# Kernel tuning notes

Measured on AMD Instinct MI355X. Metric: run time of the kernel, lower is better.

Reference implementation:

```python
import jax, jax.numpy as jnp
import numpy as np
import math

B, H, L, D = 2, 16, 2048, 128

def setup_inputs() -> dict:
    key = jax.random.key(0)
    kq, kk, kv, km = jax.random.split(key, 4)
    q = jax.random.normal(kq, (B, H, L, D), dtype=jnp.float32)
    k = jax.random.normal(kk, (B, H, L, D), dtype=jnp.float32)
    v = jax.random.normal(kv, (B, H, L, D), dtype=jnp.float32)
    mask = jax.random.randint(km, (B, 1, L, L), 0, 2, dtype=jnp.int32)
    return {"q": q, "k": k, "v": v, "mask": mask}

def reference(q, k, v, mask):
    d_tensor = q.shape[-1]
    # ReLU applied to V before attention (the custom twist)
    v = jax.nn.relu(v)
    # score = q @ k^T / sqrt(d)  -> [B,H,L,L]
    score = jnp.einsum('bhqd,bhkd->bhqk', q, k) / math.sqrt(d_tensor)
    score = jnp.where(mask == 0, jnp.float32(-10000.0), score)
    attn = jax.nn.softmax(score, axis=-1)
    # result = attn @ relu(v) -> [B,H,L,D]
    return jnp.einsum('bhqk,bhkd->bhqd', attn, v)
```

## Files before the change

### kernel.cpp

```cpp
#include <hip/hip_runtime.h>
#include <hip/hip_bf16.h>
#include <math.h>

typedef __attribute__((ext_vector_type(8)))  short short8;
typedef __attribute__((ext_vector_type(16))) float f32x16;

#define Bc    2
#define Hc    16
#define Lc    2048
#define Dc    128
#define QBLK  128
#define KBLK  64
#define LOG2E 1.4426950408889634f
#define SCALE 0.08838834764831845f
#define SCL2  (SCALE * LOG2E)

#define KB_OFF   0u
#define KB_BYTES (32u * 2048u * 128u * 2u)
#define VT_OFF   (KB_OFF + KB_BYTES)
#define VT_BYTES (32u * 2048u * 128u * 2u)
#define MB_OFF   (VT_OFF + VT_BYTES)

__device__ __forceinline__ unsigned pk2(float a, float b) {
    unsigned short ua = __builtin_bit_cast(unsigned short, __float2bfloat16(a));
    unsigned short ub = __builtin_bit_cast(unsigned short, __float2bfloat16(b));
    return (unsigned)ua | ((unsigned)ub << 16);
}
__device__ __forceinline__ unsigned short bf16b(float a) {
    return __builtin_bit_cast(unsigned short, __float2bfloat16(a));
}
__device__ __forceinline__ void gload_lds16(const void* g, void* l) {
    __builtin_amdgcn_global_load_lds(
        (const __attribute__((address_space(1))) unsigned int*)g,
        (__attribute__((address_space(3))) unsigned int*)l, 16, 0, 0);
}
__device__ __forceinline__ unsigned cvtpk(float lo, float hi) {
    unsigned r;
    asm("v_cvt_pk_bf16_f32 %0, %1, %2" : "=v"(r) : "v"(lo), "v"(hi));
    return r;
}

__global__ void prepass_kernel(const float* __restrict__ k, const float* __restrict__ v,
                               const int* __restrict__ mask,
                               unsigned short* __restrict__ kb, unsigned short* __restrict__ vt,
                               unsigned long long* __restrict__ mb) {
    __shared__ float t[32][33];
    int bid = blockIdx.x;
    int tid = threadIdx.x;
    if (bid < 4096) {
        size_t base = ((size_t)bid * 256 + tid) * 8;
        float4 f0 = *(const float4*)(k + base);
        float4 f1 = *(const float4*)(k + base + 4);
        uint4 w;
        w.x = pk2(f0.x, f0.y); w.y = pk2(f0.z, f0.w);
        w.z = pk2(f1.x, f1.y); w.w = pk2(f1.z, f1.w);
        *(uint4*)(kb + base) = w;
    } else if (bid < 12288) {
        int b2 = bid - 4096;
        int bh = b2 >> 8, rem = b2 & 255;
        int l0 = (rem >> 2) * 32, d0 = (rem & 3) * 32;
        int tx = tid & 31, ty = tid >> 5;
        const float* src = v + (size_t)bh * Lc * Dc;
        unsigned short* dst = vt + (size_t)bh * Dc * Lc;
        #pragma unroll
        for (int i = 0; i < 4; ++i) {
            int row = ty * 4 + i;
            t[row][tx] = fmaxf(src[(size_t)(l0 + row) * Dc + d0 + tx], 0.f);
        }
        __syncthreads();
        #pragma unroll
        for (int i = 0; i < 4; ++i) {
            int drow = ty * 4 + i;
            dst[(size_t)(d0 + drow) * Lc + l0 + tx] = bf16b(t[tx][drow]);
        }
    } else {
        int m = bid - 12288;
        int wv = tid >> 6, lane = tid & 63;
        #pragma unroll
        for (int i = 0; i < 16; ++i) {
            int wid = m * 64 + wv * 16 + i;
            int b = wid >> 16, l = (wid >> 5) & 2047, ktw = wid & 31;
            int mm = mask[(((size_t)(b * 2048 + l)) << 11) + ktw * 64 + lane];
            unsigned long long bal = __ballot(mm != 0);
            if (lane == 0) mb[(((size_t)(b * 32 + ktw)) << 11) + l] = bal;
        }
    }
}

__global__ __launch_bounds__(256, 2) void rev_attn_kernel(
    const float* __restrict__ q,
    const unsigned short* __restrict__ kb,
    const unsigned short* __restrict__ vt,
    const unsigned long long* __restrict__ mb,
    float* __restrict__ out)
{
    __shared__ __align__(16) char smem[65536];

    const int tid  = threadIdx.x;
    const int w    = tid >> 6;
    const int lane = tid & 63;
    const int l31  = lane & 31;
    const int hi   = lane >> 5;
    const int bh   = blockIdx.y;
    const int b    = bh >> 4;
    const int qb   = blockIdx.x * QBLK + w * 32;
    const int qrow = qb + l31;

    const float*              qp = q  + (size_t)bh * Lc * Dc;
    const unsigned short*     kp = kb + (size_t)bh * Lc * Dc;
    const unsigned short*     vp = vt + (size_t)bh * Dc * Lc;
    const unsigned long long* mp = mb + ((size_t)b << 16);
    float*                    op = out + (size_t)bh * Lc * Dc;

    short8 qf[8];
    {
        const float* qr0 = qp + (size_t)qrow * Dc + hi * 8;
        #pragma unroll
        for (int c = 0; c < 8; ++c) {
            const float* src = qr0 + c * 16;
            #pragma unroll
            for (int j = 0; j < 8; ++j)
                qf[c][j] = (short)bf16b(src[j] * SCL2);
        }
    }

    f32x16 o0 = (f32x16)0.f, o1 = (f32x16)0.f, o2 = (f32x16)0.f, o3 = (f32x16)0.f;
    f32x16 lacc = (f32x16)0.f;
    short8 ones;
    #pragma unroll
    for (int j = 0; j < 8; ++j) ones[j] = (short)0x3F80;

    #define STAGE(buf, kt_) do {                                                   \
        char* Kdst = smem + (buf) * 16384;                                         \
        char* Vdst = smem + 32768 + (buf) * 16384;                                 \
        _Pragma("unroll")                                                          \
        for (int p = 0; p < 4; ++p) {                                              \
            int l   = p * 256 + tid;                                               \
            int row = l >> 4, cl = l & 15;                                         \
            int s_  = cl ^ (row & 15);                                             \
            gload_lds16(kp + (size_t)((kt_) + row) * Dc + s_ * 8, Kdst + l * 16);  \
            int ds_ = row + ((s_ >> 3) << 6);                                      \
            int ko_ = (s_ & 7) * 8;                                                \
            gload_lds16(vp + (size_t)ds_ * Lc + (kt_) + ko_, Vdst + l * 16);       \
        }                                                                          \
    } while (0)

    #define MK_SLICE(PA, SV, J0, CS0, MREG) do {                                   \
        float e0 = ((MREG >> (CS0 + 0)) & 1u)  ? exp2f(SV[J0 + 0]) : 0.f;          \
        float e1 = ((MREG >> (CS0 + 1)) & 1u)  ? exp2f(SV[J0 + 1]) : 0.f;          \
        float e2 = ((MREG >> (CS0 + 2)) & 1u)  ? exp2f(SV[J0 + 2]) : 0.f;          \
        float e3 = ((MREG >> (CS0 + 3)) & 1u)  ? exp2f(SV[J0 + 3]) : 0.f;          \
        float e4 = ((MREG >> (CS0 + 8)) & 1u)  ? exp2f(SV[J0 + 4]) : 0.f;          \
        float e5 = ((MREG >> (CS0 + 9)) & 1u)  ? exp2f(SV[J0 + 5]) : 0.f;          \
        float e6 = ((MREG >> (CS0 + 10)) & 1u) ? exp2f(SV[J0 + 6]) : 0.f;          \
        float e7 = ((MREG >> (CS0 + 11)) & 1u) ? exp2f(SV[J0 + 7]) : 0.f;          \
        unsigned a_ = cvtpk(e0, e1), a2_ = cvtpk(e2, e3);                          \
        unsigned b_ = cvtpk(e4, e5), b2_ = cvtpk(e6, e7);                          \
        asm volatile("v_permlane32_swap_b32 %0, %1" : "+v"(a_),  "+v"(b_));        \
        asm volatile("v_permlane32_swap_b32 %0, %1" : "+v"(a2_), "+v"(b2_));       \
        union { unsigned u[4]; short8 v8; } tu_;                                   \
        tu_.u[0] = a_; tu_.u[1] = a2_; tu_.u[2] = b_; tu_.u[3] = b2_;              \
        PA = tu_.v8;                                                               \
    } while (0)

    #define PV_SLICE(PA, KS) do {                                                  \
        __builtin_amdgcn_s_setprio(1);                                             \
        lacc = __builtin_amdgcn_mfma_f32_32x32x16_bf16(ones, PA, lacc, 0, 0, 0);   \
        short8 vfa = *(const short8*)(Vb + vrowA * 256 + ((((0 << 3) | ((KS) << 1) | hi) ^ vswz) * 16)); \
        o0 = __builtin_amdgcn_mfma_f32_32x32x16_bf16(vfa, PA, o0, 0, 0, 0);        \
        short8 vfb = *(const short8*)(Vb + vrowB * 256 + ((((0 << 3) | ((KS) << 1) | hi) ^ vswz) * 16)); \
        o1 = __builtin_amdgcn_mfma_f32_32x32x16_bf16(vfb, PA, o1, 0, 0, 0);        \
        short8 vfc = *(const short8*)(Vb + vrowA * 256 + ((((1 << 3) | ((KS) << 1) | hi) ^ vswz) * 16)); \
        o2 = __builtin_amdgcn_mfma_f32_32x32x16_bf16(vfc, PA, o2, 0, 0, 0);        \
        short8 vfd = *(const short8*)(Vb + vrowB * 256 + ((((1 << 3) | ((KS) << 1) | hi) ^ vswz) * 16)); \
        o3 = __builtin_amdgcn_mfma_f32_32x32x16_bf16(vfd, PA, o3, 0, 0, 0);        \
        __builtin_amdgcn_s_setprio(0);                                             \
    } while (0)

    const int vrowA = l31;
    const int vrowB = 32 + l31;
    const int vswz  = l31 & 15;

    int cur = 0;
    STAGE(0, 0);
    asm volatile("s_waitcnt vmcnt(0)" ::: "memory");
    __builtin_amdgcn_s_barrier();
    __builtin_amdgcn_sched_barrier(0);

    for (int kt = 0; kt < Lc; kt += KBLK) {
        STAGE(cur ^ 1, (kt + KBLK) & (Lc - 1));
        unsigned long long mw = mp[((size_t)(kt >> 6) << 11) + qrow];

        asm volatile("s_waitcnt vmcnt(9)" ::: "memory");
        __builtin_amdgcn_s_barrier();
        __builtin_amdgcn_sched_barrier(0);

        const char* Kb = smem + cur * 16384;
        const char* Vb = smem + 32768 + cur * 16384;

        f32x16 s0 = (f32x16)0.f, s1 = (f32x16)0.f;
        __builtin_amdgcn_s_setprio(1);
        #pragma unroll
        for (int c = 0; c < 8; ++c) {
            int r0 = l31;
            short8 kf0 = *(const short8*)(Kb + r0 * 256 + ((((c << 1) | hi)) ^ (r0 & 15)) * 16);
            s0 = __builtin_amdgcn_mfma_f32_32x32x16_bf16(kf0, qf[c], s0, 0, 0, 0);
            int r1 = 32 + l31;
            short8 kf1 = *(const short8*)(Kb + r1 * 256 + ((((c << 1) | hi)) ^ (r1 & 15)) * 16);
            s1 = __builtin_amdgcn_mfma_f32_32x32x16_bf16(kf1, qf[c], s1, 0, 0, 0);
        }
        __builtin_amdgcn_s_setprio(0);

        unsigned m0 = ((unsigned)(mw & 0xffffffffull)) >> (4 * hi);
        unsigned m1 = ((unsigned)(mw >> 32)) >> (4 * hi);

        short8 pa;
        MK_SLICE(pa, s0, 0, 0,  m0);  PV_SLICE(pa, 0);
        MK_SLICE(pa, s0, 8, 16, m0);  PV_SLICE(pa, 1);
        MK_SLICE(pa, s1, 0, 0,  m1);  PV_SLICE(pa, 2);
        MK_SLICE(pa, s1, 8, 16, m1);  PV_SLICE(pa, 3);

        asm volatile("" ::: "memory");
        __builtin_amdgcn_s_barrier();
        __builtin_amdgcn_sched_barrier(0);
        cur ^= 1;
    }

    __syncthreads();
    float inv = 1.0f / lacc[0];
    float* scr = (float*)(smem + w * 4608);
    const int qq = lane >> 1;
    const int dh = (lane & 1) * 16;
    #pragma unroll
    for (int dt = 0; dt < 4; ++dt) {
        const f32x16& oo = (dt == 0) ? o0 : (dt == 1) ? o1 : (dt == 2) ? o2 : o3;
        #pragma unroll
        for (int r = 0; r < 16; ++r) {
            int drow = (r & 3) + 8 * (r >> 2) + 4 * hi;
            scr[drow * 36 + l31] = oo[r] * inv;
        }
        asm volatile("s_waitcnt lgkmcnt(0)" ::: "memory");
        __builtin_amdgcn_sched_barrier(0);
        float t[16];
        #pragma unroll
        for (int c2 = 0; c2 < 16; ++c2)
            t[c2] = scr[(dh + c2) * 36 + qq];
        asm volatile("s_waitcnt lgkmcnt(0)" ::: "memory");
        __builtin_amdgcn_sched_barrier(0);
        float* od = op + (size_t)(qb + qq) * Dc + dt * 32 + dh;
        #pragma unroll
        for (int c2 = 0; c2 < 4; ++c2) {
            float4 f4; f4.x = t[c2*4]; f4.y = t[c2*4+1]; f4.z = t[c2*4+2]; f4.w = t[c2*4+3];
            *(float4*)(od + c2 * 4) = f4;
        }
    }
}

extern "C" void kernel_launch(void* const* d_in, const int* in_sizes, int n_in,
                              void* d_out, int out_size, void* d_ws, size_t ws_size,
                              hipStream_t stream) {
    const float* q    = (const float*)d_in[0];
    const float* k    = (const float*)d_in[1];
    const float* v    = (const float*)d_in[2];
    const int*   mask = (const int*)d_in[3];
    float*       out  = (float*)d_out;

    char* ws = (char*)d_ws;
    unsigned short*     kb  = (unsigned short*)(ws + KB_OFF);
    unsigned short*     vt  = (unsigned short*)(ws + VT_OFF);
    unsigned long long* mbp = (unsigned long long*)(ws + MB_OFF);

    hipLaunchKernelGGL(prepass_kernel, dim3(14336), dim3(256), 0, stream, k, v, mask, kb, vt, mbp);
    hipLaunchKernelGGL(rev_attn_kernel, dim3(Lc / QBLK, Bc * Hc), dim3(256), 0, stream,
                       q, kb, vt, mbp, out);
}
```

Before: 123.3 us.

## Split each key tile across two waves per query group with 512-thread blocks

Doubles the block to 8 waves. Each pair of waves shares a 32-row query group, and each wave of the pair handles half of the 64-key tile. The partial O and row sums are combined through shared memory in the epilogue. The aim is more waves in flight and shorter per-wave dependency chains for latency hiding. In exchange it adds extra barriers and a cross-wave reduction, duplicates Q fragments in registers, and may reduce how many blocks fit per CU.

```diff
diff --git a/kernel.cpp b/kernel.cpp
--- a/kernel.cpp
+++ b/kernel.cpp
@@ -87,7 +87,7 @@
     }
 }
 
-__global__ __launch_bounds__(256, 2) void rev_attn_kernel(
+__global__ __launch_bounds__(512, 2) void rev_attn_kernel(
     const float* __restrict__ q,
     const unsigned short* __restrict__ kb,
     const unsigned short* __restrict__ vt,
@@ -101,10 +101,12 @@
     const int lane = tid & 63;
     const int l31  = lane & 31;
     const int hi   = lane >> 5;
+    const int qg   = w >> 1;
+    const int kh   = w & 1;
     const int bh   = blockIdx.y;
     const int b    = bh >> 4;
-    const int qb   = blockIdx.x * QBLK + w * 32;
-    const int qrow = qb + l31;
+    const int qb   = blockIdx.x * QBLK;
+    const int qrow = qb + qg * 32 + l31;
 
     const float*              qp = q  + (size_t)bh * Lc * Dc;
     const unsigned short*     kp = kb + (size_t)bh * Lc * Dc;
@@ -134,8 +136,8 @@
         char* Kdst = smem + (buf) * 16384;                                         \
         char* Vdst = smem + 32768 + (buf) * 16384;                                 \
         _Pragma("unroll")                                                          \
-        for (int p = 0; p < 4; ++p) {                                              \
-            int l   = p * 256 + tid;                                               \
+        for (int p = 0; p < 2; ++p) {                                              \
+            int l   = p * 512 + tid;                                               \
             int row = l >> 4, cl = l & 15;                                         \
             int s_  = cl ^ (row & 15);                                             \
             gload_lds16(kp + (size_t)((kt_) + row) * Dc + s_ * 8, Kdst + l * 16);  \
@@ -166,13 +168,13 @@
     #define PV_SLICE(PA, KS) do {                                                  \
         __builtin_amdgcn_s_setprio(1);                                             \
         lacc = __builtin_amdgcn_mfma_f32_32x32x16_bf16(ones, PA, lacc, 0, 0, 0);   \
-        short8 vfa = *(const short8*)(Vb + vrowA * 256 + ((((0 << 3) | ((KS) << 1) | hi) ^ vswz) * 16)); \
+        short8 vfa = *(const short8*)(Vb + vrowA * 256 + ((((0 << 3) | (kh << 2) | ((KS) << 1) | hi) ^ vswz) * 16)); \
         o0 = __builtin_amdgcn_mfma_f32_32x32x16_bf16(vfa, PA, o0, 0, 0, 0);        \
-        short8 vfb = *(const short8*)(Vb + vrowB * 256 + ((((0 << 3) | ((KS) << 1) | hi) ^ vswz) * 16)); \
+        short8 vfb = *(const short8*)(Vb + vrowB * 256 + ((((0 << 3) | (kh << 2) | ((KS) << 1) | hi) ^ vswz) * 16)); \
         o1 = __builtin_amdgcn_mfma_f32_32x32x16_bf16(vfb, PA, o1, 0, 0, 0);        \
-        short8 vfc = *(const short8*)(Vb + vrowA * 256 + ((((1 << 3) | ((KS) << 1) | hi) ^ vswz) * 16)); \
+        short8 vfc = *(const short8*)(Vb + vrowA * 256 + ((((1 << 3) | (kh << 2) | ((KS) << 1) | hi) ^ vswz) * 16)); \
         o2 = __builtin_amdgcn_mfma_f32_32x32x16_bf16(vfc, PA, o2, 0, 0, 0);        \
-        short8 vfd = *(const short8*)(Vb + vrowB * 256 + ((((1 << 3) | ((KS) << 1) | hi) ^ vswz) * 16)); \
+        short8 vfd = *(const short8*)(Vb + vrowB * 256 + ((((1 << 3) | (kh << 2) | ((KS) << 1) | hi) ^ vswz) * 16)); \
         o3 = __builtin_amdgcn_mfma_f32_32x32x16_bf16(vfd, PA, o3, 0, 0, 0);        \
         __builtin_amdgcn_s_setprio(0);                                             \
     } while (0)
@@ -180,6 +182,7 @@
     const int vrowA = l31;
     const int vrowB = 32 + l31;
     const int vswz  = l31 & 15;
+    const int r0    = kh * 32 + l31;
 
     int cur = 0;
     STAGE(0, 0);
@@ -191,34 +194,28 @@
         STAGE(cur ^ 1, (kt + KBLK) & (Lc - 1));
         unsigned long long mw = mp[((size_t)(kt >> 6) << 11) + qrow];
 
-        asm volatile("s_waitcnt vmcnt(9)" ::: "memory");
+        asm volatile("s_waitcnt vmcnt(5)" ::: "memory");
         __builtin_amdgcn_s_barrier();
         __builtin_amdgcn_sched_barrier(0);
 
         const char* Kb = smem + cur * 16384;
         const char* Vb = smem + 32768 + cur * 16384;
 
-        f32x16 s0 = (f32x16)0.f, s1 = (f32x16)0.f;
+        f32x16 s = (f32x16)0.f;
         __builtin_amdgcn_s_setprio(1);
         #pragma unroll
         for (int c = 0; c < 8; ++c) {
-            int r0 = l31;
-            short8 kf0 = *(const short8*)(Kb + r0 * 256 + ((((c << 1) | hi)) ^ (r0 & 15)) * 16);
-            s0 = __builtin_amdgcn_mfma_f32_32x32x16_bf16(kf0, qf[c], s0, 0, 0, 0);
-            int r1 = 32 + l31;
-            short8 kf1 = *(const short8*)(Kb + r1 * 256 + ((((c << 1) | hi)) ^ (r1 & 15)) * 16);
-            s1 = __builtin_amdgcn_mfma_f32_32x32x16_bf16(kf1, qf[c], s1, 0, 0, 0);
+            short8 kf = *(const short8*)(Kb + r0 * 256 + ((((c << 1) | hi)) ^ (r0 & 15)) * 16);
+            s = __builtin_amdgcn_mfma_f32_32x32x16_bf16(kf, qf[c], s, 0, 0, 0);
         }
         __builtin_amdgcn_s_setprio(0);
 
-        unsigned m0 = ((unsigned)(mw & 0xffffffffull)) >> (4 * hi);
-        unsigned m1 = ((unsigned)(mw >> 32)) >> (4 * hi);
+        unsigned mh = (unsigned)(mw >> (kh * 32));
+        unsigned m0 = mh >> (4 * hi);
 
         short8 pa;
-        MK_SLICE(pa, s0, 0, 0,  m0);  PV_SLICE(pa, 0);
-        MK_SLICE(pa, s0, 8, 16, m0);  PV_SLICE(pa, 1);
-        MK_SLICE(pa, s1, 0, 0,  m1);  PV_SLICE(pa, 2);
-        MK_SLICE(pa, s1, 8, 16, m1);  PV_SLICE(pa, 3);
+        MK_SLICE(pa, s, 0, 0,  m0);  PV_SLICE(pa, 0);
+        MK_SLICE(pa, s, 8, 16, m0);  PV_SLICE(pa, 1);
 
         asm volatile("" ::: "memory");
         __builtin_amdgcn_s_barrier();
@@ -227,32 +224,41 @@
     }
 
     __syncthreads();
-    float inv = 1.0f / lacc[0];
-    float* scr = (float*)(smem + w * 4608);
-    const int qq = lane >> 1;
-    const int dh = (lane & 1) * 16;
+    float* scr = (float*)(smem + qg * 4096);
+    float* lsp = (float*)(smem + 16384 + qg * 128);
+    if (kh == 1 && hi == 0) lsp[l31] = lacc[0];
+    float inv = 0.f;
+    const int qq2 = kh * 16 + (lane >> 2);
+    const int dh2 = (lane & 3) * 8;
     #pragma unroll
     for (int dt = 0; dt < 4; ++dt) {
         const f32x16& oo = (dt == 0) ? o0 : (dt == 1) ? o1 : (dt == 2) ? o2 : o3;
-        #pragma unroll
-        for (int r = 0; r < 16; ++r) {
-            int drow = (r & 3) + 8 * (r >> 2) + 4 * hi;
-            scr[drow * 36 + l31] = oo[r] * inv;
-        }
-        asm volatile("s_waitcnt lgkmcnt(0)" ::: "memory");
-        __builtin_amdgcn_sched_barrier(0);
-        float t[16];
-        #pragma unroll
-        for (int c2 = 0; c2 < 16; ++c2)
-            t[c2] = scr[(dh + c2) * 36 + qq];
-        asm volatile("s_waitcnt lgkmcnt(0)" ::: "memory");
-        __builtin_amdgcn_sched_barrier(0);
-        float* od = op + (size_t)(qb + qq) * Dc + dt * 32 + dh;
-        #pragma unroll
-        for (int c2 = 0; c2 < 4; ++c2) {
-            float4 f4; f4.x = t[c2*4]; f4.y = t[c2*4+1]; f4.z = t[c2*4+2]; f4.w = t[c2*4+3];
-            *(float4*)(od + c2 * 4) = f4;
-        }
+        if (kh == 1) {
+            #pragma unroll
+            for (int r = 0; r < 16; ++r)
+                scr[((r & 3) + 8 * (r >> 2) + 4 * hi) * 32 + l31] = oo[r];
+        }
+        __syncthreads();
+        if (kh == 0) {
+            if (dt == 0) inv = 1.0f / (lacc[0] + lsp[l31]);
+            #pragma unroll
+            for (int r = 0; r < 16; ++r) {
+                int ix = ((r & 3) + 8 * (r >> 2) + 4 * hi) * 32 + l31;
+                scr[ix] = (scr[ix] + oo[r]) * inv;
+            }
+        }
+        __syncthreads();
+        float t[8];
+        #pragma unroll
+        for (int c2 = 0; c2 < 8; ++c2)
+            t[c2] = scr[(dh2 + c2) * 32 + qq2];
+        float* od = op + (size_t)(qb + qg * 32 + qq2) * Dc + dt * 32 + dh2;
+        float4 f4a, f4b;
+        f4a.x = t[0]; f4a.y = t[1]; f4a.z = t[2]; f4a.w = t[3];
+        f4b.x = t[4]; f4b.y = t[5]; f4b.z = t[6]; f4b.w = t[7];
+        *(float4*)(od)     = f4a;
+        *(float4*)(od + 4) = f4b;
+        if (dt < 3) __syncthreads();
     }
 }
 
@@ -271,6 +277,6 @@
     unsigned long long* mbp = (unsigned long long*)(ws + MB_OFF);
 
     hipLaunchKernelGGL(prepass_kernel, dim3(14336), dim3(256), 0, stream, k, v, mask, kb, vt, mbp);
-    hipLaunchKernelGGL(rev_attn_kernel, dim3(Lc / QBLK, Bc * Hc), dim3(256), 0, stream,
+    hipLaunchKernelGGL(rev_attn_kernel, dim3(Lc / QBLK, Bc * Hc), dim3(512), 0, stream,
                        q, kb, vt, mbp, out);
 }
```

Measured after the change: 141.3 us. 14.6% more time.
